# Optimization experiments

Measured on AMD Instinct MI355X. Metric: run time of the kernel, lower is better.

Reference implementation:

```python
import jax, jax.numpy as jnp
import numpy as np
import math

NH = 12      # num attention heads
WIN = 128    # one-sided sliding window
NG = 32      # number of global (prefix) tokens
NEG = -1e9
LN_EPS = 1e-12


def _layernorm(x, g, b):
    mu = jnp.mean(x, axis=-1, keepdims=True)
    var = jnp.mean(jnp.square(x - mu), axis=-1, keepdims=True)
    return (x - mu) * jax.lax.rsqrt(var + LN_EPS) * g + b


def _longformer_self_attn(h, am, Wq, bq, Wk, bk, Wv, bv):
    B, S, D = h.shape
    Dh = D // NH
    w = WIN
    C = S // w  # number of chunks

    def proj(Wm, bm):
        return (h @ Wm + bm).reshape(B, S, NH, Dh).transpose(0, 2, 1, 3)

    q = proj(Wq, bq) * (1.0 / math.sqrt(Dh))  # [B,H,S,Dh]
    k = proj(Wk, bk)
    v = proj(Wv, bv)

    # ---- banded (sliding window) scores, chunked: each query chunk sees 3w keys ----
    kp = jnp.pad(k, ((0, 0), (0, 0), (w, w), (0, 0)))
    vp = jnp.pad(v, ((0, 0), (0, 0), (w, w), (0, 0)))
    idx = jnp.arange(C)[:, None] * w + jnp.arange(3 * w)[None, :]  # [C,3w]
    k3 = kp[:, :, idx]  # [B,H,C,3w,Dh]
    v3 = vp[:, :, idx]
    qc = q.reshape(B, NH, C, w, Dh)
    band = jnp.einsum('bhcqd,bhckd->bhcqk', qc, k3)  # [B,H,C,w,3w]

    qpos = (jnp.arange(C) * w)[:, None, None] + jnp.arange(w)[None, :, None]  # [C,w,1]
    kpos = (idx - w)[:, None, :]  # [C,1,3w] absolute key positions
    valid = (jnp.abs(kpos - qpos) <= w) & (kpos >= NG) & (kpos < S)  # band, exclude global keys

    amp = jnp.pad(am, ((0, 0), (w, w)))
    am3 = amp[:, idx]  # [B,C,3w] additive mask gathered per chunk
    band = band + am3[:, None, :, None, :]
    band = jnp.where(valid[None, None], band, NEG)
    band = band.reshape(B, NH, S, 3 * w)

    # ---- every token also attends to the NG global tokens ----
    gsc = jnp.einsum('bhsd,bhgd->bhsg', q, k[:, :, :NG]) + am[:, None, None, :NG]

    logits = jnp.concatenate([band, gsc], axis=-1)  # [B,H,S,3w+NG]
    probs = jax.nn.softmax(logits, axis=-1)
    pb = probs[..., :3 * w].reshape(B, NH, C, w, 3 * w)
    out = jnp.einsum('bhcqk,bhckd->bhcqd', pb, v3).reshape(B, NH, S, Dh)
    out = out + jnp.einsum('bhsg,bhgd->bhsd', probs[..., 3 * w:], v[:, :, :NG])

    # ---- global tokens attend to everything ----
    gl = jnp.einsum('bhgd,bhsd->bhgs', q[:, :, :NG], k) + am[:, None, None, :]
    outg = jnp.einsum('bhgs,bhsd->bhgd', jax.nn.softmax(gl, axis=-1), v)

    ctx = jnp.concatenate([outg, out[:, :, NG:]], axis=2)  # [B,H,S,Dh]
    return ctx.transpose(0, 2, 1, 3).reshape(B, S, D)


def setup_inputs() -> dict:
    key = jax.random.key(0)
    ks = jax.random.split(key, 8)
    B, S, D, F = 2, 4096, 768, 3072
    p = lambda k_, sh: jax.random.normal(k_, sh, jnp.float32) * 0.02
    return {
        'hidden_states': jax.random.normal(ks[0], (B, S, D), jnp.float32),
        'attention_mask': jnp.zeros((B, S), jnp.float32),
        'Wq': p(ks[1], (D, D)), 'bq': jnp.zeros((D,), jnp.float32),
        'Wk': p(ks[2], (D, D)), 'bk': jnp.zeros((D,), jnp.float32),
        'Wv': p(ks[3], (D, D)), 'bv': jnp.zeros((D,), jnp.float32),
        'Wo': p(ks[4], (D, D)), 'bo': jnp.zeros((D,), jnp.float32),
        'ln1_g': jnp.ones((D,), jnp.float32), 'ln1_b': jnp.zeros((D,), jnp.float32),
        'Wi': p(ks[5], (D, F)), 'bi': jnp.zeros((F,), jnp.float32),
        'Wo2': p(ks[6], (F, D)), 'bo2': jnp.zeros((D,), jnp.float32),
        'ln2_g': jnp.ones((D,), jnp.float32), 'ln2_b': jnp.zeros((D,), jnp.float32),
    }


def reference(hidden_states, attention_mask, Wq, bq, Wk, bk, Wv, bv, Wo, bo,
              ln1_g, ln1_b, Wi, bi, Wo2, bo2, ln2_g, ln2_b):
    ctx = _longformer_self_attn(hidden_states, attention_mask, Wq, bq, Wk, bk, Wv, bv)
    attn_out = _layernorm(ctx @ Wo + bo + hidden_states, ln1_g, ln1_b)
    inter = jax.nn.gelu(attn_out @ Wi + bi, approximate=False)
    layer_out = _layernorm(inter @ Wo2 + bo2 + attn_out, ln2_g, ln2_b)
    return layer_out
```

## Files before the change

### kernel.cpp

```cpp
#include <hip/hip_runtime.h>
#include <math.h>

#define NHEAD 12
#define DH 64
#define S_LEN 4096
#define B_SZ 2
#define D_MODEL 768
#define FF_DIM 3072
#define WINSZ 128
#define NGLB 32
#define NEGV -1e9f
#define NQC 6291456L

typedef __attribute__((ext_vector_type(8))) short bf16x8;
typedef __attribute__((ext_vector_type(4))) float floatx4;

__device__ __forceinline__ unsigned short f2bf(float x) {
    union { float f; unsigned u; } v; v.f = x;
    unsigned r = v.u + 0x7fffu + ((v.u >> 16) & 1u);
    return (unsigned short)(r >> 16);
}
__device__ __forceinline__ float bf2f(unsigned short x) {
    union { unsigned u; float f; } v; v.u = ((unsigned)x) << 16;
    return v.f;
}

__device__ __forceinline__ void async_copy16(const unsigned short* g, unsigned short* l) {
    __builtin_amdgcn_global_load_lds(
        (const __attribute__((address_space(1))) void*)g,
        (__attribute__((address_space(3))) void*)l, 16, 0, 0);
}

__global__ __launch_bounds__(256) void prep_k(
    const float* __restrict__ Wq, const float* __restrict__ Wk,
    const float* __restrict__ Wv, const float* __restrict__ Wo,
    const float* __restrict__ Wi, const float* __restrict__ Wo2,
    unsigned short* __restrict__ wqt, unsigned short* __restrict__ wkt,
    unsigned short* __restrict__ wvt, unsigned short* __restrict__ wot,
    unsigned short* __restrict__ wit, unsigned short* __restrict__ wo2t,
    const float* __restrict__ bq, const float* __restrict__ bk,
    const float* __restrict__ bv, float* __restrict__ bcat,
    const float* __restrict__ hid, unsigned short* __restrict__ hidb)
{
    __shared__ float tile[32][33];
    const int bid = blockIdx.x;
    const int tx = threadIdx.x, ty = threadIdx.y;

    if (bid < 6912) {
        const float* src; unsigned short* dst; int K, N, nx, local; float scale = 1.f;
        if (bid < 576)       { src = Wq;  dst = wqt;  K = 768;  N = 768;  nx = 24; local = bid;        scale = 0.125f; }
        else if (bid < 1152) { src = Wk;  dst = wkt;  K = 768;  N = 768;  nx = 24; local = bid - 576;  }
        else if (bid < 1728) { src = Wv;  dst = wvt;  K = 768;  N = 768;  nx = 24; local = bid - 1152; }
        else if (bid < 2304) { src = Wo;  dst = wot;  K = 768;  N = 768;  nx = 24; local = bid - 1728; }
        else if (bid < 4608) { src = Wi;  dst = wit;  K = 768;  N = 3072; nx = 96; local = bid - 2304; }
        else                 { src = Wo2; dst = wo2t; K = 3072; N = 768;  nx = 24; local = bid - 4608; }
        const int n0 = (local % nx) * 32, k0 = (local / nx) * 32;
#pragma unroll
        for (int i = 0; i < 4; ++i)
            tile[ty + 8 * i][tx] = src[(long)(k0 + ty + 8 * i) * N + n0 + tx];
        __syncthreads();
#pragma unroll
        for (int i = 0; i < 4; ++i)
            dst[(long)(n0 + ty + 8 * i) * K + k0 + tx] = f2bf(tile[tx][ty + 8 * i] * scale);
    } else if (bid < 6921) {
        const int t = ty * 32 + tx;
        const int i = (bid - 6912) * 256 + t;
        if (i < 768) bcat[i] = bq[i] * 0.125f;
        else if (i < 1536) bcat[i] = bk[i - 768];
        else if (i < 2304) bcat[i] = bv[i - 1536];
    } else {
        const int t = ty * 32 + tx;
        const long i = ((long)(bid - 6921) * 256 + t) * 4;
        float4 v = *(const float4*)(hid + i);
        ushort4 o;
        o.x = f2bf(v.x); o.y = f2bf(v.y); o.z = f2bf(v.z); o.w = f2bf(v.w);
        *(ushort4*)(hidb + i) = o;
    }
}

__global__ __launch_bounds__(256) void vt_k(
    const unsigned short* __restrict__ v, unsigned short* __restrict__ vt)
{
    const int bh = blockIdx.y;
    const int s0 = blockIdx.x * 32;
    const int w = threadIdx.x >> 6, lane = threadIdx.x & 63;
    const unsigned short* src = v + ((long)bh * S_LEN + s0 + w * 8) * DH + lane;
    unsigned short r[8];
#pragma unroll
    for (int j = 0; j < 8; ++j) r[j] = src[j * DH];
    unsigned short* dst = vt + ((long)bh * DH + lane) * S_LEN + s0 + w * 8;
    ushort4 lo, hi;
    lo.x = r[0]; lo.y = r[1]; lo.z = r[2]; lo.w = r[3];
    hi.x = r[4]; hi.y = r[5]; hi.z = r[6]; hi.w = r[7];
    *(ushort4*)dst = lo;
    *(ushort4*)(dst + 4) = hi;
}

#define GEMM_BODY(U, PF, TAILW)                                              \
    {                                                                        \
        if (PF) {                                                            \
            async_copy16(aSrc0 + (U + 2) * 32, &As[(U + 2) % 3][g0]);        \
            async_copy16(bSrc0 + (U + 2) * 32, &Bs[(U + 2) % 3][g0]);        \
            async_copy16(aSrc1 + (U + 2) * 32, &As[(U + 2) % 3][g1]);        \
            async_copy16(bSrc1 + (U + 2) * 32, &Bs[(U + 2) % 3][g1]);        \
        }                                                                    \
        __builtin_amdgcn_sched_barrier(0);                                   \
        bf16x8 af[4], bfr[4];                                                \
        _Pragma("unroll")                                                    \
        for (int i = 0; i < 4; ++i) {                                        \
            af[i]  = *(const bf16x8*)&As[U][rdA + i * 512];                  \
            bfr[i] = *(const bf16x8*)&Bs[U][rdB + i * 512];                  \
        }                                                                    \
        __builtin_amdgcn_s_setprio(1);                                       \
        _Pragma("unroll")                                                    \
        for (int i = 0; i < 4; ++i)                                          \
            _Pragma("unroll")                                                \
            for (int j = 0; j < 4; ++j)                                      \
                acc[i][j] = __builtin_amdgcn_mfma_f32_16x16x32_bf16(         \
                    af[i], bfr[j], acc[i][j], 0, 0, 0);                      \
        __builtin_amdgcn_s_setprio(0);                                       \
        __builtin_amdgcn_sched_barrier(0);                                   \
        if (TAILW == 2) {                                                    \
            asm volatile("s_waitcnt vmcnt(4)" ::: "memory");                 \
            __builtin_amdgcn_s_barrier();                                    \
        } else if (TAILW == 1) {                                             \
            asm volatile("s_waitcnt vmcnt(0)" ::: "memory");                 \
            __builtin_amdgcn_s_barrier();                                    \
        }                                                                    \
        __builtin_amdgcn_sched_barrier(0);                                   \
    }

template <int EPI>
__global__ __launch_bounds__(256) void gemm_bf(
    const unsigned short* __restrict__ A, const unsigned short* __restrict__ BT,
    const float* __restrict__ bias, void* __restrict__ out,
    int M, int N, int K, int nx)
{
    __shared__ unsigned short As[3][128 * 32];
    __shared__ unsigned short Bs[3][128 * 32];
    const int tid = threadIdx.x;
    const int wave = tid >> 6, lane = tid & 63;
    const int t8 = (blockIdx.x & 7) * (gridDim.x >> 3) + (blockIdx.x >> 3);
    const int m0 = (t8 / nx) * 128, n0 = (t8 % nx) * 128;
    const int wr = (wave >> 1) * 64, wc = (wave & 1) * 64;

    floatx4 acc[4][4];
#pragma unroll
    for (int i = 0; i < 4; ++i)
#pragma unroll
        for (int j = 0; j < 4; ++j) acc[i][j] = (floatx4){0.f, 0.f, 0.f, 0.f};

    const int srow = lane >> 2;
    const int schk = (((lane & 3) ^ (srow & 3))) * 8;
    const int r = lane & 15;
    const int q8 = ((lane >> 4) ^ (lane & 3)) * 8;
    const int rdA = (wr + r) * 32 + q8;
    const int rdB = (wc + r) * 32 + q8;

    const int NT = K >> 5;
    const unsigned short* aSrc0 = A  + (long)(m0 + wave * 32 + srow) * K + schk;
    const unsigned short* aSrc1 = A  + (long)(m0 + wave * 32 + 16 + srow) * K + schk;
    const unsigned short* bSrc0 = BT + (long)(n0 + wave * 32 + srow) * K + schk;
    const unsigned short* bSrc1 = BT + (long)(n0 + wave * 32 + 16 + srow) * K + schk;
    const int g0 = wave * 1024, g1 = wave * 1024 + 512;

    async_copy16(aSrc0, &As[0][g0]);
    async_copy16(bSrc0, &Bs[0][g0]);
    async_copy16(aSrc1, &As[0][g1]);
    async_copy16(bSrc1, &Bs[0][g1]);
    async_copy16(aSrc0 + 32, &As[1][g0]);
    async_copy16(bSrc0 + 32, &Bs[1][g0]);
    async_copy16(aSrc1 + 32, &As[1][g1]);
    async_copy16(bSrc1 + 32, &Bs[1][g1]);
    asm volatile("s_waitcnt vmcnt(4)" ::: "memory");
    __builtin_amdgcn_s_barrier();
    __builtin_amdgcn_sched_barrier(0);

    for (int t3 = 0; t3 < NT - 3; t3 += 3) {
        GEMM_BODY(0, 1, 2)
        GEMM_BODY(1, 1, 2)
        GEMM_BODY(2, 1, 2)
        aSrc0 += 96; aSrc1 += 96; bSrc0 += 96; bSrc1 += 96;
    }
    GEMM_BODY(0, 1, 2)
    GEMM_BODY(1, 0, 1)
    GEMM_BODY(2, 0, 0)

    const int col_l = lane & 15, row_l = (lane >> 4) * 4;
#pragma unroll
    for (int i = 0; i < 4; ++i) {
#pragma unroll
        for (int j = 0; j < 4; ++j) {
            const int n = n0 + wc + j * 16 + col_l;
            const float bv = bias[n];
#pragma unroll
            for (int rg = 0; rg < 4; ++rg) {
                const int m = m0 + wr + i * 16 + row_l + rg;
                float v = acc[i][j][rg] + bv;
                if (EPI == 1) {
                    v = 0.5f * v * (1.f + erff(v * 0.70710678118654752f));
                    ((unsigned short*)out)[(long)m * N + n] = f2bf(v);
                } else {
                    const int bb = m >> 12, s = m & 4095;
                    const int part = n / 768;
                    const int nn = n - part * 768;
                    const int hh = nn >> 6, dh = nn & 63;
                    ((unsigned short*)out)[(long)part * NQC +
                        (((long)bb * NHEAD + hh) * S_LEN + s) * DH + dh] = f2bf(v);
                }
            }
        }
    }
}

__global__ __launch_bounds__(256) void gemm_sp(
    const unsigned short* __restrict__ A, const unsigned short* __restrict__ BT,
    float* __restrict__ p0, float* __restrict__ p1,
    int M, int N, int K2, int nx, int ntile)
{
    __shared__ unsigned short As[3][128 * 32];
    __shared__ unsigned short Bs[3][128 * 32];
    const int tid = threadIdx.x;
    const int wave = tid >> 6, lane = tid & 63;
    const int t8 = (blockIdx.x & 7) * (gridDim.x >> 3) + (blockIdx.x >> 3);
    const int slice = t8 >= ntile;
    const int tile = t8 - slice * ntile;
    const int m0 = (tile / nx) * 128, n0 = (tile % nx) * 128;
    const int kbeg = slice * K2;
    float* P = slice ? p1 : p0;
    const int wr = (wave >> 1) * 64, wc = (wave & 1) * 64;

    floatx4 acc[4][4];
#pragma unroll
    for (int i = 0; i < 4; ++i)
#pragma unroll
        for (int j = 0; j < 4; ++j) acc[i][j] = (floatx4){0.f, 0.f, 0.f, 0.f};

    const int srow = lane >> 2;
    const int schk = (((lane & 3) ^ (srow & 3))) * 8;
    const int r = lane & 15;
    const int q8 = ((lane >> 4) ^ (lane & 3)) * 8;
    const int rdA = (wr + r) * 32 + q8;
    const int rdB = (wc + r) * 32 + q8;
    const long Kl = (long)K2 * 2;

    const int NT = K2 >> 5;
    const unsigned short* aSrc0 = A  + (long)(m0 + wave * 32 + srow) * Kl + kbeg + schk;
    const unsigned short* aSrc1 = A  + (long)(m0 + wave * 32 + 16 + srow) * Kl + kbeg + schk;
    const unsigned short* bSrc0 = BT + (long)(n0 + wave * 32 + srow) * Kl + kbeg + schk;
    const unsigned short* bSrc1 = BT + (long)(n0 + wave * 32 + 16 + srow) * Kl + kbeg + schk;
    const int g0 = wave * 1024, g1 = wave * 1024 + 512;

    async_copy16(aSrc0, &As[0][g0]);
    async_copy16(bSrc0, &Bs[0][g0]);
    async_copy16(aSrc1, &As[0][g1]);
    async_copy16(bSrc1, &Bs[0][g1]);
    async_copy16(aSrc0 + 32, &As[1][g0]);
    async_copy16(bSrc0 + 32, &Bs[1][g0]);
    async_copy16(aSrc1 + 32, &As[1][g1]);
    async_copy16(bSrc1 + 32, &Bs[1][g1]);
    asm volatile("s_waitcnt vmcnt(4)" ::: "memory");
    __builtin_amdgcn_s_barrier();
    __builtin_amdgcn_sched_barrier(0);

    for (int t3 = 0; t3 < NT - 3; t3 += 3) {
        GEMM_BODY(0, 1, 2)
        GEMM_BODY(1, 1, 2)
        GEMM_BODY(2, 1, 2)
        aSrc0 += 96; aSrc1 += 96; bSrc0 += 96; bSrc1 += 96;
    }
    GEMM_BODY(0, 1, 2)
    GEMM_BODY(1, 0, 1)
    GEMM_BODY(2, 0, 0)

    const int col_l = lane & 15, row_l = (lane >> 4) * 4;
#pragma unroll
    for (int i = 0; i < 4; ++i)
#pragma unroll
        for (int j = 0; j < 4; ++j) {
            const int n = n0 + wc + j * 16 + col_l;
#pragma unroll
            for (int rg = 0; rg < 4; ++rg) {
                const int m = m0 + wr + i * 16 + row_l + rg;
                P[(long)m * N + n] = acc[i][j][rg];
            }
        }
}

__global__ __launch_bounds__(256) void attn_k(
    const unsigned short* __restrict__ q, const unsigned short* __restrict__ k,
    const unsigned short* __restrict__ vt, const float* __restrict__ am,
    unsigned short* __restrict__ ctx)
{
    __shared__ __align__(16) unsigned char smem[28800];
    const int blk = blockIdx.x;
    const int tid = threadIdx.x;
    const int wave = tid >> 6, lane = tid & 63;
    const int ln15 = lane & 15, ln4 = lane >> 4;

    if (blk >= 24) {
        unsigned short* Ks = (unsigned short*)smem;
        unsigned short* Vs = Ks + 32 * 72;
        unsigned short* Ps = Vs + 64 * 40;

        const int bb = blk - 24;
        const int c = bb & 31;
        const int h = (bb >> 5) % NHEAD;
        const int b = bb / (32 * NHEAD);
        const long bh = (long)b * NHEAD + h;

        const unsigned short* kh  = k + bh * S_LEN * DH;
        const unsigned short* vth = vt + bh * (long)DH * S_LEN;
        const float* amb = am + (long)b * S_LEN;

        const int q0 = c * WINSZ + wave * 32;

        bf16x8 qf[2][2];
#pragma unroll
        for (int nt = 0; nt < 2; ++nt)
#pragma unroll
            for (int ks = 0; ks < 2; ++ks)
                qf[nt][ks] = *(const bf16x8*)(q + (bh * S_LEN + q0 + nt * 16 + ln15) * DH
                                              + ks * 32 + ln4 * 8);

        floatx4 o[4][2];
#pragma unroll
        for (int mt = 0; mt < 4; ++mt)
#pragma unroll
            for (int nt = 0; nt < 2; ++nt) o[mt][nt] = (floatx4){0.f, 0.f, 0.f, 0.f};
        float m_r[2] = {-1e30f, -1e30f}, l_r[2] = {0.f, 0.f};

        const int sk_key = tid >> 3, sk_ch = tid & 7;
        const int sv_dim = tid & 63, sv_ch = tid >> 6;
        const bf16x8 zero8 = {0, 0, 0, 0, 0, 0, 0, 0};

        for (int tile = 0; tile < 13; ++tile) {
            const bool glob = (tile == 12);
            const int kbase = glob ? 0 : (c * WINSZ - WINSZ + tile * 32);

            __syncthreads();
            {
                int kpos = kbase + sk_key;
                bf16x8 val = zero8;
                if ((unsigned)kpos < (unsigned)S_LEN)
                    val = *(const bf16x8*)(kh + (long)kpos * DH + sk_ch * 8);
                *(bf16x8*)(&Ks[sk_key * 72 + sk_ch * 8]) = val;
            }
            {
                int kc = kbase + sv_ch * 8;
                bf16x8 val = zero8;
                if (kc >= 0 && kc + 8 <= S_LEN)
                    val = *(const bf16x8*)(vth + (long)sv_dim * S_LEN + kc);
                *(bf16x8*)(&Vs[sv_dim * 40 + sv_ch * 8]) = val;
            }
            __syncthreads();

            bf16x8 ak[2][2];
#pragma unroll
            for (int mt = 0; mt < 2; ++mt)
#pragma unroll
                for (int ks = 0; ks < 2; ++ks)
                    ak[mt][ks] = *(const bf16x8*)(&Ks[(mt * 16 + ln15) * 72 + ks * 32 + ln4 * 8]);

            floatx4 s[2][2];
#pragma unroll
            for (int mt = 0; mt < 2; ++mt)
#pragma unroll
                for (int nt = 0; nt < 2; ++nt) {
                    floatx4 acc = (floatx4){0.f, 0.f, 0.f, 0.f};
                    acc = __builtin_amdgcn_mfma_f32_16x16x32_bf16(ak[mt][0], qf[nt][0], acc, 0, 0, 0);
                    acc = __builtin_amdgcn_mfma_f32_16x16x32_bf16(ak[mt][1], qf[nt][1], acc, 0, 0, 0);
                    s[mt][nt] = acc;
                }

#pragma unroll
            for (int mt = 0; mt < 2; ++mt) {
                const int kp0 = kbase + mt * 16 + ln4 * 4;
#pragma unroll
                for (int rg = 0; rg < 4; ++rg) {
                    const int kpos = kp0 + rg;
                    const bool kin = (unsigned)kpos < (unsigned)S_LEN;
                    const float amv = kin ? amb[kpos] : 0.f;
#pragma unroll
                    for (int nt = 0; nt < 2; ++nt) {
                        const int qpos = q0 + nt * 16 + ln15;
                        const int dlt = kpos > qpos ? kpos - qpos : qpos - kpos;
                        const bool valid = glob || (kpos >= NGLB && kin && dlt <= WINSZ);
                        s[mt][nt][rg] = valid ? s[mt][nt][rg] + amv : NEGV;
                    }
                }
            }

            float alpha[2];
#pragma unroll
            for (int nt = 0; nt < 2; ++nt) {
                float mx = s[0][nt][0];
#pragma unroll
                for (int rg = 1; rg < 4; ++rg) mx = fmaxf(mx, s[0][nt][rg]);
#pragma unroll
                for (int rg = 0; rg < 4; ++rg) mx = fmaxf(mx, s[1][nt][rg]);
                mx = fmaxf(mx, __shfl_xor(mx, 16));
                mx = fmaxf(mx, __shfl_xor(mx, 32));
                const float mn = fmaxf(m_r[nt], mx);
                alpha[nt] = __expf(m_r[nt] - mn);
                m_r[nt] = mn;
            }

#pragma unroll
            for (int nt = 0; nt < 2; ++nt) {
                float sum = 0.f;
#pragma unroll
                for (int mt = 0; mt < 2; ++mt) {
                    ushort4 pk;
#pragma unroll
                    for (int rg = 0; rg < 4; ++rg) {
                        const float p = __expf(s[mt][nt][rg] - m_r[nt]);
                        sum += p;
                        ((unsigned short*)&pk)[rg] = f2bf(p);
                    }
                    *(ushort4*)(&Ps[wave * 1280 + (nt * 16 + ln15) * 40 + mt * 16 + ln4 * 4]) = pk;
                }
                sum += __shfl_xor(sum, 16);
                sum += __shfl_xor(sum, 32);
                l_r[nt] = l_r[nt] * alpha[nt] + sum;
            }

#pragma unroll
            for (int mt = 0; mt < 4; ++mt)
#pragma unroll
                for (int nt = 0; nt < 2; ++nt)
#pragma unroll
                    for (int rg = 0; rg < 4; ++rg) o[mt][nt][rg] *= alpha[nt];

            bf16x8 av[4], bp[2];
#pragma unroll
            for (int mt = 0; mt < 4; ++mt)
                av[mt] = *(const bf16x8*)(&Vs[(mt * 16 + ln15) * 40 + ln4 * 8]);
#pragma unroll
            for (int nt = 0; nt < 2; ++nt)
                bp[nt] = *(const bf16x8*)(&Ps[wave * 1280 + (nt * 16 + ln15) * 40 + ln4 * 8]);
#pragma unroll
            for (int mt = 0; mt < 4; ++mt)
#pragma unroll
                for (int nt = 0; nt < 2; ++nt)
                    o[mt][nt] = __builtin_amdgcn_mfma_f32_16x16x32_bf16(
                        av[mt], bp[nt], o[mt][nt], 0, 0, 0);
        }

        if (q0 >= NGLB) {
            const float inv0 = 1.f / l_r[0], inv1 = 1.f / l_r[1];
#pragma unroll
            for (int nt = 0; nt < 2; ++nt) {
                const float inv = nt ? inv1 : inv0;
                const long row = (long)b * S_LEN + q0 + nt * 16 + ln15;
#pragma unroll
                for (int mt = 0; mt < 4; ++mt) {
                    ushort4 ov;
#pragma unroll
                    for (int rg = 0; rg < 4; ++rg)
                        ((unsigned short*)&ov)[rg] = f2bf(o[mt][nt][rg] * inv);
                    *(ushort4*)(ctx + row * D_MODEL + h * DH + mt * 16 + ln4 * 4) = ov;
                }
            }
        }
    } else {
        unsigned short* Psg = (unsigned short*)smem;
        float* Om   = (float*)(smem + 18432);
        float* mW   = (float*)(smem + 27648);
        float* lW   = (float*)(smem + 28160);
        float* lTot = (float*)(smem + 28672);

        const int bh = blk;
        const int b = bh / NHEAD, h = bh % NHEAD;

        const unsigned short* kh  = k + (long)bh * S_LEN * DH;
        const unsigned short* vth = vt + (long)bh * DH * S_LEN;
        const float* amb = am + (long)b * S_LEN;

        bf16x8 qf[2][2];
#pragma unroll
        for (int nt = 0; nt < 2; ++nt)
#pragma unroll
            for (int ks = 0; ks < 2; ++ks)
                qf[nt][ks] = *(const bf16x8*)(q + ((long)bh * S_LEN + nt * 16 + ln15) * DH
                                              + ks * 32 + ln4 * 8);

        floatx4 o[4][2];
#pragma unroll
        for (int mt = 0; mt < 4; ++mt)
#pragma unroll
            for (int nt = 0; nt < 2; ++nt) o[mt][nt] = (floatx4){0.f, 0.f, 0.f, 0.f};
        float m_r[2] = {-1e30f, -1e30f}, l_r[2] = {0.f, 0.f};

        for (int it = 0; it < 16; ++it) {
            const int kbase = it * 256 + wave * 64;

            bf16x8 ak[4][2];
#pragma unroll
            for (int mt = 0; mt < 4; ++mt)
#pragma unroll
                for (int ks = 0; ks < 2; ++ks)
                    ak[mt][ks] = *(const bf16x8*)(kh + (long)(kbase + mt * 16 + ln15) * DH
                                                  + ks * 32 + ln4 * 8);

            floatx4 s[4][2];
#pragma unroll
            for (int mt = 0; mt < 4; ++mt)
#pragma unroll
                for (int nt = 0; nt < 2; ++nt) {
                    floatx4 acc = (floatx4){0.f, 0.f, 0.f, 0.f};
                    acc = __builtin_amdgcn_mfma_f32_16x16x32_bf16(ak[mt][0], qf[nt][0], acc, 0, 0, 0);
                    acc = __builtin_amdgcn_mfma_f32_16x16x32_bf16(ak[mt][1], qf[nt][1], acc, 0, 0, 0);
                    s[mt][nt] = acc;
                }

#pragma unroll
            for (int mt = 0; mt < 4; ++mt) {
                const int kp0 = kbase + mt * 16 + ln4 * 4;
#pragma unroll
                for (int rg = 0; rg < 4; ++rg) {
                    const float amv = amb[kp0 + rg];
#pragma unroll
                    for (int nt = 0; nt < 2; ++nt) s[mt][nt][rg] += amv;
                }
            }

            float alpha[2];
#pragma unroll
            for (int nt = 0; nt < 2; ++nt) {
                float mx = s[0][nt][0];
#pragma unroll
                for (int mt = 0; mt < 4; ++mt)
#pragma unroll
                    for (int rg = 0; rg < 4; ++rg) mx = fmaxf(mx, s[mt][nt][rg]);
                mx = fmaxf(mx, __shfl_xor(mx, 16));
                mx = fmaxf(mx, __shfl_xor(mx, 32));
                const float mn = fmaxf(m_r[nt], mx);
                alpha[nt] = __expf(m_r[nt] - mn);
                m_r[nt] = mn;
            }

#pragma unroll
            for (int nt = 0; nt < 2; ++nt) {
                float sum = 0.f;
#pragma unroll
                for (int mt = 0; mt < 4; ++mt) {
                    ushort4 pk;
#pragma unroll
                    for (int rg = 0; rg < 4; ++rg) {
                        const float p = __expf(s[mt][nt][rg] - m_r[nt]);
                        sum += p;
                        ((unsigned short*)&pk)[rg] = f2bf(p);
                    }
                    *(ushort4*)(&Psg[wave * 2304 + (nt * 16 + ln15) * 72 + mt * 16 + ln4 * 4]) = pk;
                }
                sum += __shfl_xor(sum, 16);
                sum += __shfl_xor(sum, 32);
                l_r[nt] = l_r[nt] * alpha[nt] + sum;
            }

#pragma unroll
            for (int mt = 0; mt < 4; ++mt)
#pragma unroll
                for (int nt = 0; nt < 2; ++nt)
#pragma unroll
                    for (int rg = 0; rg < 4; ++rg) o[mt][nt][rg] *= alpha[nt];

            bf16x8 av[4][2], bp[2][2];
#pragma unroll
            for (int mt = 0; mt < 4; ++mt)
#pragma unroll
                for (int ks = 0; ks < 2; ++ks)
                    av[mt][ks] = *(const bf16x8*)(vth + (long)(mt * 16 + ln15) * S_LEN
                                                  + kbase + ks * 32 + ln4 * 8);
#pragma unroll
            for (int nt = 0; nt < 2; ++nt)
#pragma unroll
                for (int ks = 0; ks < 2; ++ks)
                    bp[nt][ks] = *(const bf16x8*)(&Psg[wave * 2304 + (nt * 16 + ln15) * 72
                                                  + ks * 32 + ln4 * 8]);
#pragma unroll
            for (int mt = 0; mt < 4; ++mt)
#pragma unroll
                for (int nt = 0; nt < 2; ++nt) {
                    o[mt][nt] = __builtin_amdgcn_mfma_f32_16x16x32_bf16(
                        av[mt][0], bp[nt][0], o[mt][nt], 0, 0, 0);
                    o[mt][nt] = __builtin_amdgcn_mfma_f32_16x16x32_bf16(
                        av[mt][1], bp[nt][1], o[mt][nt], 0, 0, 0);
                }
        }

        if (ln4 == 0) {
#pragma unroll
            for (int nt = 0; nt < 2; ++nt) {
                mW[wave * 32 + nt * 16 + ln15] = m_r[nt];
                lW[wave * 32 + nt * 16 + ln15] = l_r[nt];
            }
        }
        for (int i = tid; i < 64 * 36; i += 256) Om[i] = 0.f;
        __syncthreads();

        float f[2];
#pragma unroll
        for (int nt = 0; nt < 2; ++nt) {
            const int qq = nt * 16 + ln15;
            float mt_ = mW[qq];
#pragma unroll
            for (int w = 1; w < 4; ++w) mt_ = fmaxf(mt_, mW[w * 32 + qq]);
            float lt = 0.f;
#pragma unroll
            for (int w = 0; w < 4; ++w) lt += __expf(mW[w * 32 + qq] - mt_) * lW[w * 32 + qq];
            f[nt] = __expf(m_r[nt] - mt_);
            if (wave == 0 && ln4 == 0) lTot[qq] = lt;
        }
#pragma unroll
        for (int mt = 0; mt < 4; ++mt)
#pragma unroll
            for (int nt = 0; nt < 2; ++nt)
#pragma unroll
                for (int rg = 0; rg < 4; ++rg) o[mt][nt][rg] *= f[nt];

        for (int wv = 0; wv < 4; ++wv) {
            if (wave == wv) {
#pragma unroll
                for (int mt = 0; mt < 4; ++mt)
#pragma unroll
                    for (int nt = 0; nt < 2; ++nt)
#pragma unroll
                        for (int rg = 0; rg < 4; ++rg)
                            Om[(mt * 16 + ln4 * 4 + rg) * 36 + nt * 16 + ln15] += o[mt][nt][rg];
            }
            __syncthreads();
        }

        const int qq = tid >> 3, d0 = (tid & 7) * 8;
        const float inv = 1.f / lTot[qq];
        ushort4 ov0, ov1;
#pragma unroll
        for (int i = 0; i < 4; ++i)
            ((unsigned short*)&ov0)[i] = f2bf(Om[(d0 + i) * 36 + qq] * inv);
#pragma unroll
        for (int i = 0; i < 4; ++i)
            ((unsigned short*)&ov1)[i] = f2bf(Om[(d0 + 4 + i) * 36 + qq] * inv);
        unsigned short* dst = ctx + ((long)b * S_LEN + qq) * D_MODEL + h * DH + d0;
        *(ushort4*)dst = ov0;
        *(ushort4*)(dst + 4) = ov1;
    }
}

__global__ __launch_bounds__(256) void ln2p_k(
    const float* __restrict__ p0, const float* __restrict__ p1,
    const float* __restrict__ bias, const float* __restrict__ resid,
    float* __restrict__ out, unsigned short* __restrict__ out_bf,
    const float* __restrict__ gw, const float* __restrict__ bw)
{
    __shared__ float red[8];
    const long base = (long)blockIdx.x * D_MODEL;
    const int t = threadIdx.x;
    const int wv = t >> 6, lane = t & 63;
    float v0 = p0[base + t]       + p1[base + t]       + bias[t]       + resid[base + t];
    float v1 = p0[base + t + 256] + p1[base + t + 256] + bias[t + 256] + resid[base + t + 256];
    float v2 = p0[base + t + 512] + p1[base + t + 512] + bias[t + 512] + resid[base + t + 512];

    float s = v0 + v1 + v2;
#pragma unroll
    for (int off = 32; off; off >>= 1) s += __shfl_xor(s, off);
    if (lane == 0) red[wv] = s;
    __syncthreads();
    const float mu = (red[0] + red[1] + red[2] + red[3]) * (1.f / 768.f);

    const float d0 = v0 - mu, d1 = v1 - mu, d2 = v2 - mu;
    float s2 = d0 * d0 + d1 * d1 + d2 * d2;
#pragma unroll
    for (int off = 32; off; off >>= 1) s2 += __shfl_xor(s2, off);
    if (lane == 0) red[4 + wv] = s2;
    __syncthreads();
    const float var = (red[4] + red[5] + red[6] + red[7]) * (1.f / 768.f);
    const float rs = rsqrtf(var + 1e-12f);

    const float y0 = d0 * rs * gw[t] + bw[t];
    const float y1 = d1 * rs * gw[t + 256] + bw[t + 256];
    const float y2 = d2 * rs * gw[t + 512] + bw[t + 512];
    if (out) {
        float* y = out + base;
        y[t] = y0; y[t + 256] = y1; y[t + 512] = y2;
    }
    if (out_bf) {
        unsigned short* yb = out_bf + base;
        yb[t] = f2bf(y0); yb[t + 256] = f2bf(y1); yb[t + 512] = f2bf(y2);
    }
}

extern "C" void kernel_launch(void* const* d_in, const int* in_sizes, int n_in,
                              void* d_out, int out_size, void* d_ws, size_t ws_size,
                              hipStream_t stream)
{
    const float* hid  = (const float*)d_in[0];
    const float* am   = (const float*)d_in[1];
    const float* Wq   = (const float*)d_in[2];
    const float* bq   = (const float*)d_in[3];
    const float* Wk   = (const float*)d_in[4];
    const float* bk   = (const float*)d_in[5];
    const float* Wv   = (const float*)d_in[6];
    const float* bv   = (const float*)d_in[7];
    const float* Wo   = (const float*)d_in[8];
    const float* bo   = (const float*)d_in[9];
    const float* ln1g = (const float*)d_in[10];
    const float* ln1b = (const float*)d_in[11];
    const float* Wi   = (const float*)d_in[12];
    const float* bi   = (const float*)d_in[13];
    const float* Wo2  = (const float*)d_in[14];
    const float* bo2  = (const float*)d_in[15];
    const float* ln2g = (const float*)d_in[16];
    const float* ln2b = (const float*)d_in[17];

    const long M  = (long)B_SZ * S_LEN;
    const long NQ = NQC;

    unsigned short* W16 = (unsigned short*)d_ws;
    unsigned short* qb   = W16;
    unsigned short* kb   = W16 + NQ;
    unsigned short* vb   = W16 + 2 * NQ;
    unsigned short* vtb  = W16 + 3 * NQ;
    unsigned short* ctxb = W16 + 4 * NQ;
    unsigned short* hidb = W16 + 5 * NQ;
    unsigned short* wqt  = W16 + 6 * NQ;
    unsigned short* wkt  = wqt + 589824;
    unsigned short* wvt  = wkt + 589824;
    unsigned short* wot  = wvt + 589824;
    unsigned short* wit  = wot + 589824;
    unsigned short* wo2t = wit + 2359296;
    float* tmp   = (float*)(W16 + 44826624);
    float* partB1 = (float*)(W16 + 57409536);
    float* bcat  = (float*)(W16 + 69992448);
    float* partA0 = (float*)W16;
    float* partA1 = (float*)(W16 + 2 * NQ);
    unsigned short* interb = W16;
    unsigned short* attnb  = hidb;
    float* partB0 = (float*)(W16 + 4 * NQ);
    (void)ws_size; (void)in_sizes; (void)n_in; (void)out_size;

    prep_k<<<dim3(13065), dim3(32, 8), 0, stream>>>(
        Wq, Wk, Wv, Wo, Wi, Wo2, wqt, wkt, wvt, wot, wit, wo2t,
        bq, bk, bv, bcat, hid, hidb);

    dim3 blk(256);

    gemm_bf<2><<<dim3(1152), blk, 0, stream>>>(hidb, wqt, bcat, qb,
                                               M, 2304, 768, 18);

    vt_k<<<dim3(128, 24), blk, 0, stream>>>(vb, vtb);

    attn_k<<<dim3(792), blk, 0, stream>>>(qb, kb, vtb, am, ctxb);

    gemm_sp<<<dim3(768), blk, 0, stream>>>(ctxb, wot, partA0, partA1,
                                           M, 768, 384, 6, 384);
    ln2p_k<<<dim3(M), blk, 0, stream>>>(partA0, partA1, bo, hid,
                                        tmp, attnb, ln1g, ln1b);

    gemm_bf<1><<<dim3(1536), blk, 0, stream>>>(attnb, wit, bi, interb,
                                               M, 3072, 768, 24);

    gemm_sp<<<dim3(768), blk, 0, stream>>>(interb, wo2t, partB0, partB1,
                                           M, 768, 1536, 6, 384);
    ln2p_k<<<dim3(M), blk, 0, stream>>>(partB0, partB1, bo2, tmp,
                                        (float*)d_out, nullptr, ln2g, ln2b);
}
```

Baseline: 405.2 us.

## Load GEMM B operand directly from global into registers, drop B LDS staging

```diff
diff --git a/kernel.cpp b/kernel.cpp
--- a/kernel.cpp
+++ b/kernel.cpp
@@ -96,35 +96,37 @@
     *(ushort4*)(dst + 4) = hi;
 }
 
-#define GEMM_BODY(U, PF, TAILW)                                              \
+#define GB(U, BC, BN, PFA, PFB, WN)                                          \
     {                                                                        \
-        if (PF) {                                                            \
+        if (PFA) {                                                           \
             async_copy16(aSrc0 + (U + 2) * 32, &As[(U + 2) % 3][g0]);        \
-            async_copy16(bSrc0 + (U + 2) * 32, &Bs[(U + 2) % 3][g0]);        \
             async_copy16(aSrc1 + (U + 2) * 32, &As[(U + 2) % 3][g1]);        \
-            async_copy16(bSrc1 + (U + 2) * 32, &Bs[(U + 2) % 3][g1]);        \
+        }                                                                    \
+        if (PFB) {                                                           \
+            BN[0] = *(const bf16x8*)(bP0 + (U + 1) * 32);                    \
+            BN[1] = *(const bf16x8*)(bP1 + (U + 1) * 32);                    \
+            BN[2] = *(const bf16x8*)(bP2 + (U + 1) * 32);                    \
+            BN[3] = *(const bf16x8*)(bP3 + (U + 1) * 32);                    \
         }                                                                    \
         __builtin_amdgcn_sched_barrier(0);                                   \
-        bf16x8 af[4], bfr[4];                                                \
+        bf16x8 af[4];                                                        \
         _Pragma("unroll")                                                    \
-        for (int i = 0; i < 4; ++i) {                                        \
-            af[i]  = *(const bf16x8*)&As[U][rdA + i * 512];                  \
-            bfr[i] = *(const bf16x8*)&Bs[U][rdB + i * 512];                  \
-        }                                                                    \
+        for (int i = 0; i < 4; ++i)                                          \
+            af[i] = *(const bf16x8*)&As[(U) % 3][rdA + i * 512];             \
         __builtin_amdgcn_s_setprio(1);                                       \
         _Pragma("unroll")                                                    \
         for (int i = 0; i < 4; ++i)                                          \
             _Pragma("unroll")                                                \
             for (int j = 0; j < 4; ++j)                                      \
                 acc[i][j] = __builtin_amdgcn_mfma_f32_16x16x32_bf16(         \
-                    af[i], bfr[j], acc[i][j], 0, 0, 0);                      \
+                    af[i], BC[j], acc[i][j], 0, 0, 0);                       \
         __builtin_amdgcn_s_setprio(0);                                       \
         __builtin_amdgcn_sched_barrier(0);                                   \
-        if (TAILW == 2) {                                                    \
+        if (WN == 6) {                                                       \
+            asm volatile("s_waitcnt vmcnt(6)" ::: "memory");                 \
+            __builtin_amdgcn_s_barrier();                                    \
+        } else if (WN == 4) {                                                \
             asm volatile("s_waitcnt vmcnt(4)" ::: "memory");                 \
-            __builtin_amdgcn_s_barrier();                                    \
-        } else if (TAILW == 1) {                                             \
-            asm volatile("s_waitcnt vmcnt(0)" ::: "memory");                 \
             __builtin_amdgcn_s_barrier();                                    \
         }                                                                    \
         __builtin_amdgcn_sched_barrier(0);                                   \
@@ -137,7 +139,6 @@
     int M, int N, int K, int nx)
 {
     __shared__ unsigned short As[3][128 * 32];
-    __shared__ unsigned short Bs[3][128 * 32];
     const int tid = threadIdx.x;
     const int wave = tid >> 6, lane = tid & 63;
     const int t8 = (blockIdx.x & 7) * (gridDim.x >> 3) + (blockIdx.x >> 3);
@@ -152,39 +153,49 @@
 
     const int srow = lane >> 2;
     const int schk = (((lane & 3) ^ (srow & 3))) * 8;
-    const int r = lane & 15;
-    const int q8 = ((lane >> 4) ^ (lane & 3)) * 8;
+    const int r = lane & 15, ln4 = lane >> 4;
+    const int q8 = (ln4 ^ (lane & 3)) * 8;
     const int rdA = (wr + r) * 32 + q8;
-    const int rdB = (wc + r) * 32 + q8;
 
     const int NT = K >> 5;
-    const unsigned short* aSrc0 = A  + (long)(m0 + wave * 32 + srow) * K + schk;
-    const unsigned short* aSrc1 = A  + (long)(m0 + wave * 32 + 16 + srow) * K + schk;
-    const unsigned short* bSrc0 = BT + (long)(n0 + wave * 32 + srow) * K + schk;
-    const unsigned short* bSrc1 = BT + (long)(n0 + wave * 32 + 16 + srow) * K + schk;
+    const unsigned short* aSrc0 = A + (long)(m0 + wave * 32 + srow) * K + schk;
+    const unsigned short* aSrc1 = A + (long)(m0 + wave * 32 + 16 + srow) * K + schk;
+    const unsigned short* bP0 = BT + (long)(n0 + wc +  0 + r) * K + ln4 * 8;
+    const unsigned short* bP1 = BT + (long)(n0 + wc + 16 + r) * K + ln4 * 8;
+    const unsigned short* bP2 = BT + (long)(n0 + wc + 32 + r) * K + ln4 * 8;
+    const unsigned short* bP3 = BT + (long)(n0 + wc + 48 + r) * K + ln4 * 8;
     const int g0 = wave * 1024, g1 = wave * 1024 + 512;
 
+    bf16x8 b0[4], b1[4];
+
     async_copy16(aSrc0, &As[0][g0]);
-    async_copy16(bSrc0, &Bs[0][g0]);
     async_copy16(aSrc1, &As[0][g1]);
-    async_copy16(bSrc1, &Bs[0][g1]);
     async_copy16(aSrc0 + 32, &As[1][g0]);
-    async_copy16(bSrc0 + 32, &Bs[1][g0]);
     async_copy16(aSrc1 + 32, &As[1][g1]);
-    async_copy16(bSrc1 + 32, &Bs[1][g1]);
-    asm volatile("s_waitcnt vmcnt(4)" ::: "memory");
+    b0[0] = *(const bf16x8*)bP0;
+    b0[1] = *(const bf16x8*)bP1;
+    b0[2] = *(const bf16x8*)bP2;
+    b0[3] = *(const bf16x8*)bP3;
+    asm volatile("s_waitcnt vmcnt(6)" ::: "memory");
     __builtin_amdgcn_s_barrier();
     __builtin_amdgcn_sched_barrier(0);
 
-    for (int t3 = 0; t3 < NT - 3; t3 += 3) {
-        GEMM_BODY(0, 1, 2)
-        GEMM_BODY(1, 1, 2)
-        GEMM_BODY(2, 1, 2)
-        aSrc0 += 96; aSrc1 += 96; bSrc0 += 96; bSrc1 += 96;
+    for (int t6 = 0; t6 < NT - 6; t6 += 6) {
+        GB(0, b0, b1, 1, 1, 6)
+        GB(1, b1, b0, 1, 1, 6)
+        GB(2, b0, b1, 1, 1, 6)
+        GB(3, b1, b0, 1, 1, 6)
+        GB(4, b0, b1, 1, 1, 6)
+        GB(5, b1, b0, 1, 1, 6)
+        aSrc0 += 192; aSrc1 += 192;
+        bP0 += 192; bP1 += 192; bP2 += 192; bP3 += 192;
     }
-    GEMM_BODY(0, 1, 2)
-    GEMM_BODY(1, 0, 1)
-    GEMM_BODY(2, 0, 0)
+    GB(0, b0, b1, 1, 1, 6)
+    GB(1, b1, b0, 1, 1, 6)
+    GB(2, b0, b1, 1, 1, 6)
+    GB(3, b1, b0, 1, 1, 6)
+    GB(4, b0, b1, 0, 1, 4)
+    GB(5, b1, b0, 0, 0, 0)
 
     const int col_l = lane & 15, row_l = (lane >> 4) * 4;
 #pragma unroll
@@ -219,7 +230,6 @@
     int M, int N, int K2, int nx, int ntile)
 {
     __shared__ unsigned short As[3][128 * 32];
-    __shared__ unsigned short Bs[3][128 * 32];
     const int tid = threadIdx.x;
     const int wave = tid >> 6, lane = tid & 63;
     const int t8 = (blockIdx.x & 7) * (gridDim.x >> 3) + (blockIdx.x >> 3);
@@ -238,40 +248,50 @@
 
     const int srow = lane >> 2;
     const int schk = (((lane & 3) ^ (srow & 3))) * 8;
-    const int r = lane & 15;
-    const int q8 = ((lane >> 4) ^ (lane & 3)) * 8;
+    const int r = lane & 15, ln4 = lane >> 4;
+    const int q8 = (ln4 ^ (lane & 3)) * 8;
     const int rdA = (wr + r) * 32 + q8;
-    const int rdB = (wc + r) * 32 + q8;
     const long Kl = (long)K2 * 2;
 
     const int NT = K2 >> 5;
-    const unsigned short* aSrc0 = A  + (long)(m0 + wave * 32 + srow) * Kl + kbeg + schk;
-    const unsigned short* aSrc1 = A  + (long)(m0 + wave * 32 + 16 + srow) * Kl + kbeg + schk;
-    const unsigned short* bSrc0 = BT + (long)(n0 + wave * 32 + srow) * Kl + kbeg + schk;
-    const unsigned short* bSrc1 = BT + (long)(n0 + wave * 32 + 16 + srow) * Kl + kbeg + schk;
+    const unsigned short* aSrc0 = A + (long)(m0 + wave * 32 + srow) * Kl + kbeg + schk;
+    const unsigned short* aSrc1 = A + (long)(m0 + wave * 32 + 16 + srow) * Kl + kbeg + schk;
+    const unsigned short* bP0 = BT + (long)(n0 + wc +  0 + r) * Kl + kbeg + ln4 * 8;
+    const unsigned short* bP1 = BT + (long)(n0 + wc + 16 + r) * Kl + kbeg + ln4 * 8;
+    const unsigned short* bP2 = BT + (long)(n0 + wc + 32 + r) * Kl + kbeg + ln4 * 8;
+    const unsigned short* bP3 = BT + (long)(n0 + wc + 48 + r) * Kl + kbeg + ln4 * 8;
     const int g0 = wave * 1024, g1 = wave * 1024 + 512;
 
+    bf16x8 b0[4], b1[4];
+
     async_copy16(aSrc0, &As[0][g0]);
-    async_copy16(bSrc0, &Bs[0][g0]);
     async_copy16(aSrc1, &As[0][g1]);
-    async_copy16(bSrc1, &Bs[0][g1]);
     async_copy16(aSrc0 + 32, &As[1][g0]);
-    async_copy16(bSrc0 + 32, &Bs[1][g0]);
     async_copy16(aSrc1 + 32, &As[1][g1]);
-    async_copy16(bSrc1 + 32, &Bs[1][g1]);
-    asm volatile("s_waitcnt vmcnt(4)" ::: "memory");
+    b0[0] = *(const bf16x8*)bP0;
+    b0[1] = *(const bf16x8*)bP1;
+    b0[2] = *(const bf16x8*)bP2;
+    b0[3] = *(const bf16x8*)bP3;
+    asm volatile("s_waitcnt vmcnt(6)" ::: "memory");
     __builtin_amdgcn_s_barrier();
     __builtin_amdgcn_sched_barrier(0);
 
-    for (int t3 = 0; t3 < NT - 3; t3 += 3) {
-        GEMM_BODY(0, 1, 2)
-        GEMM_BODY(1, 1, 2)
-        GEMM_BODY(2, 1, 2)
-        aSrc0 += 96; aSrc1 += 96; bSrc0 += 96; bSrc1 += 96;
+    for (int t6 = 0; t6 < NT - 6; t6 += 6) {
+        GB(0, b0, b1, 1, 1, 6)
+        GB(1, b1, b0, 1, 1, 6)
+        GB(2, b0, b1, 1, 1, 6)
+        GB(3, b1, b0, 1, 1, 6)
+        GB(4, b0, b1, 1, 1, 6)
+        GB(5, b1, b0, 1, 1, 6)
+        aSrc0 += 192; aSrc1 += 192;
+        bP0 += 192; bP1 += 192; bP2 += 192; bP3 += 192;
     }
-    GEMM_BODY(0, 1, 2)
-    GEMM_BODY(1, 0, 1)
-    GEMM_BODY(2, 0, 0)
+    GB(0, b0, b1, 1, 1, 6)
+    GB(1, b1, b0, 1, 1, 6)
+    GB(2, b0, b1, 1, 1, 6)
+    GB(3, b1, b0, 1, 1, 6)
+    GB(4, b0, b1, 0, 1, 4)
+    GB(5, b1, b0, 0, 0, 0)
 
     const int col_l = lane & 15, row_l = (lane >> 4) * 4;
 #pragma unroll
```

Result: slower. 516.6 us (+27.5%).
